# Performance work log

Measured on AMD Instinct MI355X. Metric: run time of the kernel, lower is better.

The kernel has to match this reference:

```python
import jax, jax.numpy as jnp
import numpy as np

N, C, H = 256, 128, 4
EPS = 1e-5


def setup_inputs() -> dict:
    key = jax.random.key(0)
    ks = jax.random.split(key, 12)
    def w(k, shape):
        return jax.random.normal(k, shape, jnp.float32) * 0.02
    return {
        'pair_rep': jax.random.normal(ks[0], (N, N, C), jnp.float32),
        'single_rep': jax.random.normal(ks[1], (N, C), jnp.float32),
        'mask': jax.random.randint(ks[2], (N, N), 0, 2) == 1,
        'distance_matrix': jax.random.normal(ks[3], (N, N), jnp.float32),
        'row_Wqkv': w(ks[4], (C, 3 * C)), 'row_bqkv': jnp.zeros((3 * C,), jnp.float32),
        'row_Wo': w(ks[5], (C, C)), 'row_bo': jnp.zeros((C,), jnp.float32),
        'row_dscale': jnp.ones((1,), jnp.float32),
        'col_Wqkv': w(ks[6], (C, 3 * C)), 'col_bqkv': jnp.zeros((3 * C,), jnp.float32),
        'col_Wo': w(ks[7], (C, C)), 'col_bo': jnp.zeros((C,), jnp.float32),
        'col_dscale': jnp.ones((1,), jnp.float32),
        'pnr_g': jnp.ones((C,), jnp.float32), 'pnr_b': jnp.zeros((C,), jnp.float32),
        'pnc_g': jnp.ones((C,), jnp.float32), 'pnc_b': jnp.zeros((C,), jnp.float32),
        'sn_g': jnp.ones((C,), jnp.float32), 'sn_b': jnp.zeros((C,), jnp.float32),
        'W1': w(ks[8], (C, 2 * C)), 'b1': jnp.zeros((2 * C,), jnp.float32),
        'W2': w(ks[9], (2 * C, C)), 'b2': jnp.zeros((C,), jnp.float32),
    }


def layer_norm(x, g, b):
    m = jnp.mean(x, axis=-1, keepdims=True)
    v = jnp.mean((x - m) ** 2, axis=-1, keepdims=True)
    return (x - m) / jnp.sqrt(v + EPS) * g + b


def tri_update_out(pair, single):
    # out[i,j] = single[j] + sum_{k<i} pair[i,k]  (exclusive prefix over own row, at index i)
    n = pair.shape[0]
    cs = jnp.cumsum(pair, axis=1)                       # cs[i,j] = sum_{k<=j} pair[i,k]
    idx = jnp.arange(n)
    s = cs[idx, jnp.maximum(idx - 1, 0)]                # [n,c]
    s = jnp.where((idx > 0)[:, None], s, 0.0)
    return single[None, :, :] + s[:, None, :]


def tri_update_in(pair, single):
    # out[i,j] = single[i] + sum_{k<j} pair[k,j]
    n = pair.shape[0]
    cs = jnp.cumsum(pair, axis=0)                       # cs[i,j] = sum_{k<=i} pair[k,j]
    idx = jnp.arange(n)
    s = cs[jnp.maximum(idx - 1, 0), idx]                # [n,c]
    s = jnp.where((idx > 0)[:, None], s, 0.0)
    return single[:, None, :] + s[None, :, :]


def tri_attn(x, Wqkv, bqkv, Wo, bo, dscale, mask, dist):
    n = x.shape[0]
    d = C // H
    qkv = x @ Wqkv + bqkv                               # [n,n,3c]
    q, k, v = jnp.split(qkv, 3, axis=-1)
    q = q.reshape(n, n, H, d)
    k = k.reshape(n, n, H, d)
    v = v.reshape(n, n, H, d)
    scores = jnp.einsum('ijhd,ikhd->hijk', q, k) / np.sqrt(d).astype(np.float32)
    scores = scores + (dscale[0] * dist)[None, None, :, :]
    scores = jnp.where(mask[None, None, :, :], -jnp.inf, scores)
    w = jax.nn.softmax(scores, axis=-1)
    out = jnp.einsum('hijk,ikhd->ijhd', w, v).reshape(n, n, C)
    return out @ Wo + bo


def reference(pair_rep, single_rep, mask, distance_matrix,
              row_Wqkv, row_bqkv, row_Wo, row_bo, row_dscale,
              col_Wqkv, col_bqkv, col_Wo, col_bo, col_dscale,
              pnr_g, pnr_b, pnc_g, pnc_b, sn_g, sn_b,
              W1, b1, W2, b2):
    pr = layer_norm(pair_rep + tri_update_out(pair_rep, single_rep), pnr_g, pnr_b)
    pr = layer_norm(pr + tri_attn(pr, row_Wqkv, row_bqkv, row_Wo, row_bo, row_dscale, mask, distance_matrix), pnr_g, pnr_b)
    pr = layer_norm(pr + tri_update_in(pr, single_rep), pnc_g, pnc_b)
    pr = layer_norm(pr + tri_attn(pr, col_Wqkv, col_bqkv, col_Wo, col_bo, col_dscale, mask.T, distance_matrix), pnc_g, pnc_b)
    h = jax.nn.relu(single_rep @ W1 + b1)
    h = jax.nn.relu(h @ W2 + b2)
    sr = layer_norm(single_rep + h, sn_g, sn_b)
    return pr, sr
```

## Files before the change

kernel.cpp:

```cpp
#include <hip/hip_runtime.h>
#include <math.h>

typedef unsigned int u32;
typedef unsigned short u16;
typedef __attribute__((ext_vector_type(8))) short short8;
typedef __attribute__((ext_vector_type(4))) float f32x4;
typedef __attribute__((ext_vector_type(2))) u32 u32x2;

#define NN 256
#define CC 128
#define EPSV 1e-5f
#define LOG2E 1.44269504088896f
#define QSCL (0.17677669529663687f * 1.44269504088896f)
#define NEGBIG -1e30f

#define MFMA(a,b,c) __builtin_amdgcn_mfma_f32_16x16x32_bf16(a,b,c,0,0,0)
#define EXP2(x) __builtin_amdgcn_exp2f(x)

__device__ __forceinline__ float b2f(u16 u){ return __uint_as_float(((u32)u)<<16); }
__device__ __forceinline__ u16 f2b(float f){
  u32 x = __float_as_uint(f);
  return (u16)((x + 0x7fffu + ((x>>16)&1u)) >> 16);
}
__device__ __forceinline__ void unpk(u32 u, float&a, float&b){
  a = __uint_as_float(u<<16); b = __uint_as_float(u & 0xffff0000u);
}
__device__ __forceinline__ u32 cvtpk(float lo, float hi){
  u32 r;
  asm("v_cvt_pk_bf16_f32 %0, %1, %2" : "=v"(r) : "v"(lo), "v"(hi));
  return r;
}

#define XS_OFF   0
#define WT_OFF   65536
#define WO_OFF   90112
#define KB_OFF   100352
#define VT_OFF   120832
#define PB_OFF   138752
#define SV_OFF   159232
#define GB_OFF   159744
#define SMEM_BYTES 161280

#define XBYTE(r,c) ((r)*256 + (((((c)>>3)) ^ ((r)&7))<<4) + ((c)&7)*2)

__global__ void bias_kernel(const int* __restrict__ mask, const float* __restrict__ dist,
                            const float* __restrict__ rd, const float* __restrict__ cd,
                            u16* __restrict__ b0, u16* __restrict__ b1){
  int j = blockIdx.x, k = threadIdx.x;
  float dv = dist[j*NN + k];
  b0[j*NN + k] = mask[j*NN + k] ? f2b(NEGBIG) : f2b(rd[0]*LOG2E*dv);
  b1[j*NN + k] = mask[k*NN + j] ? f2b(NEGBIG) : f2b(cd[0]*LOG2E*dv);
}

template<int PHASE, int BIASWS>
__launch_bounds__(1024, 4)
__global__ void stage_kernel(const float* __restrict__ pin, const float* __restrict__ colmat,
                             const float* __restrict__ singlerow,
                             const int* __restrict__ mask, const float* __restrict__ dist,
                             const u16* __restrict__ biasbuf,
                             const float* __restrict__ Wqkv, const float* __restrict__ bqkv,
                             const float* __restrict__ Wo, const float* __restrict__ bo,
                             const float* __restrict__ dscale,
                             const float* __restrict__ lng, const float* __restrict__ lnb,
                             float* __restrict__ outp)
{
  extern __shared__ char smem[];
  char* Xs  = smem + XS_OFF;
  char* WTs = smem + WT_OFF;
  char* WOs = smem + WO_OFF;
  char* KBs = smem + KB_OFF;
  char* VTs = smem + VT_OFF;
  float* SVs = (float*)(smem + SV_OFF);
  float* GBs = (float*)(smem + GB_OFF);

  const int i = blockIdx.x;
  const int tid = threadIdx.x;
  const int lid = tid & 63;
  const int w = tid >> 6;
  const int l15 = lid & 15;
  const int l4  = lid >> 4;
  char* pbB = smem + PB_OFF + w*1280;
  const float dsc = dscale[0] * LOG2E;
  const float* prow = pin + (size_t)i*NN*CC;
  float* orow = outp + (size_t)i*NN*CC;
  const int qglob = w*16 + l15;

  if (tid < CC){ GBs[tid] = lng[tid]; GBs[CC+tid] = lnb[tid]; GBs[2*CC+tid] = bo[tid]; }
  if (PHASE == 0) {
    float* REDp = (float*)(smem + PB_OFF);
    int c = tid & 127, part = tid >> 7;
    float acc = 0.f;
    for (int k = part; k < i; k += 8) acc += prow[k*CC + c];
    REDp[tid] = acc;
    __syncthreads();
    if (tid < CC){
      float s = 0.f;
      #pragma unroll
      for (int p = 0; p < 8; ++p) s += REDp[p*CC + tid];
      SVs[tid] = s;
    }
  } else {
    if (tid < CC) SVs[tid] = singlerow[i*CC + tid];
  }
  __syncthreads();

  for (int r = w; r < NN; r += 16){
    float t0 = prow[r*CC + lid]      + colmat[r*CC + lid]      + SVs[lid];
    float t1 = prow[r*CC + 64 + lid] + colmat[r*CC + 64 + lid] + SVs[64 + lid];
    float s = t0 + t1, q2 = t0*t0 + t1*t1;
    #pragma unroll
    for (int ms = 1; ms < 64; ms <<= 1){ s += __shfl_xor(s, ms); q2 += __shfl_xor(q2, ms); }
    float mean = s*(1.f/CC);
    float var  = fmaxf(q2*(1.f/CC) - mean*mean, 0.f);
    float rstd = rsqrtf(var + EPSV);
    *(u16*)(Xs + XBYTE(r, lid))    = f2b((t0-mean)*rstd*GBs[lid]    + GBs[CC+lid]);
    *(u16*)(Xs + XBYTE(r, 64+lid)) = f2b((t1-mean)*rstd*GBs[64+lid] + GBs[CC+64+lid]);
  }

  f32x4 pa[8];
  #pragma unroll
  for (int ct=0;ct<8;++ct) pa[ct] = f32x4{0.f,0.f,0.f,0.f};

  for (int h = 0; h < 4; ++h){
    __syncthreads();

    #pragma unroll
    for (int it = 0; it < 12; ++it){
      int e = tid + it*1024;
      int c = e & 127, t = e >> 7;
      int col = (t < 32) ? (h*32 + t) : (t < 64) ? (CC + h*32 + (t-32)) : (2*CC + h*32 + (t-64));
      *(u16*)(WTs + t*256 + ((((c>>3) ^ (t&7)))<<4) + (c&7)*2) = f2b(Wqkv[c*384 + col]);
    }
    #pragma unroll
    for (int it = 0; it < 4; ++it){
      int e = tid + it*1024;
      int d = e >> 7, o = e & 127;
      *(u16*)(WOs + (o*40 + d)*2) = f2b(Wo[(h*32 + d)*128 + o]);
    }
    __syncthreads();

    f32x4 qa[2], ka[2], va[2];
    {
      float bq0 = bqkv[h*32 + l15],      bq1 = bqkv[h*32 + 16 + l15];
      float bk0 = bqkv[CC + h*32 + l15], bk1 = bqkv[CC + h*32 + 16 + l15];
      qa[0] = f32x4{bq0,bq0,bq0,bq0}; qa[1] = f32x4{bq1,bq1,bq1,bq1};
      ka[0] = f32x4{bk0,bk0,bk0,bk0}; ka[1] = f32x4{bk1,bk1,bk1,bk1};
      #pragma unroll
      for (int dt=0;dt<2;++dt)
        #pragma unroll
        for (int v=0;v<4;++v) va[dt][v] = bqkv[2*CC + h*32 + dt*16 + l4*4 + v];
    }
    #pragma unroll
    for (int ks = 0; ks < 4; ++ks){
      int swb = (((ks*4 + l4) ^ (l15 & 7)) << 4);
      short8 a0  = *(const short8*)(Xs  + (w*16 + l15)*256 + swb);
      short8 wq0 = *(const short8*)(WTs + (l15)*256 + swb);
      short8 wq1 = *(const short8*)(WTs + (16 + l15)*256 + swb);
      short8 wk0 = *(const short8*)(WTs + (32 + l15)*256 + swb);
      short8 wk1 = *(const short8*)(WTs + (48 + l15)*256 + swb);
      short8 wv0 = *(const short8*)(WTs + (64 + l15)*256 + swb);
      short8 wv1 = *(const short8*)(WTs + (80 + l15)*256 + swb);
      qa[0]=MFMA(a0,wq0,qa[0]); qa[1]=MFMA(a0,wq1,qa[1]);
      ka[0]=MFMA(a0,wk0,ka[0]); ka[1]=MFMA(a0,wk1,ka[1]);
      va[0]=MFMA(wv0,a0,va[0]); va[1]=MFMA(wv1,a0,va[1]);
    }
    #pragma unroll
    for (int ct=0;ct<2;++ct)
      #pragma unroll
      for (int v=0;v<4;++v){
        *(u16*)(KBs + ((w*16 + l4*4 + v)*40 + ct*16 + l15)*2) = f2b(ka[ct][v]);
        *(u16*)(pbB + ((l4*4 + v)*40 + ct*16 + l15)*2) = f2b(qa[ct][v]*QSCL);
        *(u16*)(VTs + ((ct*16 + l4*4 + v)*280 + w*16 + l15)*2) = f2b(va[ct][v]);
      }
    asm volatile("s_waitcnt lgkmcnt(0)" ::: "memory");
    short8 qf = *(const short8*)(pbB + (l15)*80 + l4*16);
    __syncthreads();

    float m = -3e38f, l = 0.f;
    f32x4 oacc[2];
    oacc[0] = f32x4{0.f,0.f,0.f,0.f}; oacc[1] = oacc[0];

    #pragma unroll
    for (int ch = 0; ch < 8; ++ch){
      const int kbase = ch*32;
      float bia[2][4];
      if (BIASWS){
        u32x2 bw0 = *(const u32x2*)(biasbuf + qglob*NN + kbase + l4*4);
        u32x2 bw1 = *(const u32x2*)(biasbuf + qglob*NN + kbase + 16 + l4*4);
        unpk(bw0.x, bia[0][0], bia[0][1]); unpk(bw0.y, bia[0][2], bia[0][3]);
        unpk(bw1.x, bia[1][0], bia[1][1]); unpk(bw1.y, bia[1][2], bia[1][3]);
      } else {
        #pragma unroll
        for (int kt=0;kt<2;++kt)
          #pragma unroll
          for (int v=0;v<4;++v){
            int ky = kbase + kt*16 + l4*4 + v;
            int mq = (PHASE==0) ? mask[qglob*NN + ky] : mask[ky*NN + qglob];
            bia[kt][v] = mq ? NEGBIG : dsc*dist[qglob*NN + ky];
          }
      }
      short8 kf0 = *(const short8*)(KBs + (kbase + l15)*80 + l4*16);
      short8 kf1 = *(const short8*)(KBs + (kbase + 16 + l15)*80 + l4*16);
      f32x4 z = f32x4{0.f,0.f,0.f,0.f};
      f32x4 s0 = MFMA(kf0, qf, z);
      f32x4 s1 = MFMA(kf1, qf, z);
      float sv0 = s0[0]+bia[0][0], sv1 = s0[1]+bia[0][1], sv2 = s0[2]+bia[0][2], sv3 = s0[3]+bia[0][3];
      float sv4 = s1[0]+bia[1][0], sv5 = s1[1]+bia[1][1], sv6 = s1[2]+bia[1][2], sv7 = s1[3]+bia[1][3];
      float mx = fmaxf(fmaxf(fmaxf(sv0,sv1),fmaxf(sv2,sv3)), fmaxf(fmaxf(sv4,sv5),fmaxf(sv6,sv7)));
      mx = fmaxf(mx, __shfl_xor(mx, 16));
      mx = fmaxf(mx, __shfl_xor(mx, 32));
      float mn = fmaxf(m, mx);
      float corr = EXP2(m - mn);
      m = mn;
      float p00 = EXP2(sv0 - m), p01 = EXP2(sv1 - m), p02 = EXP2(sv2 - m), p03 = EXP2(sv3 - m);
      float p10 = EXP2(sv4 - m), p11 = EXP2(sv5 - m), p12 = EXP2(sv6 - m), p13 = EXP2(sv7 - m);
      float ps = ((p00+p01)+(p02+p03)) + ((p10+p11)+(p12+p13));
      ps += __shfl_xor(ps, 16);
      ps += __shfl_xor(ps, 32);
      l = l*corr + ps;
      #pragma unroll
      for (int v=0;v<4;++v){ oacc[0][v] *= corr; oacc[1][v] *= corr; }
      u32 A0 = cvtpk(p00,p01), A1 = cvtpk(p02,p03);
      u32 B0 = cvtpk(p10,p11), B1 = cvtpk(p12,p13);
      asm volatile("v_permlane32_swap_b32 %0, %1" : "+v"(A0), "+v"(B0));
      asm volatile("v_permlane32_swap_b32 %0, %1" : "+v"(A1), "+v"(B1));
      u32 sA0 = __shfl_xor(A0, 16), sA1 = __shfl_xor(A1, 16);
      u32 sB0 = __shfl_xor(B0, 16), sB1 = __shfl_xor(B1, 16);
      bool eg = ((l4 & 1) == 0);
      union { u32 u[4]; short8 s; } pu;
      pu.u[0] = eg ? A0 : sB0;
      pu.u[1] = eg ? A1 : sB1;
      pu.u[2] = eg ? sA0 : B0;
      pu.u[3] = eg ? sA1 : B1;
      short8 pf = pu.s;
      short8 vt0 = *(const short8*)(VTs + (l15)*560      + (kbase + l4*8)*2);
      short8 vt1 = *(const short8*)(VTs + (16 + l15)*560 + (kbase + l4*8)*2);
      oacc[0] = MFMA(vt0, pf, oacc[0]);
      oacc[1] = MFMA(vt1, pf, oacc[1]);
    }

    {
      float inv = 1.f / l;
      #pragma unroll
      for (int dt=0;dt<2;++dt)
        #pragma unroll
        for (int v=0;v<4;++v)
          *(u16*)(pbB + (l15*40 + dt*16 + l4*4 + v)*2) = f2b(oacc[dt][v]*inv);
      asm volatile("s_waitcnt lgkmcnt(0)" ::: "memory");
      short8 oA = *(const short8*)(pbB + (l15)*80 + l4*16);
      #pragma unroll
      for (int ct=0; ct<8; ++ct){
        short8 wB = *(const short8*)(WOs + (ct*16 + l15)*80 + l4*16);
        pa[ct] = MFMA(oA, wB, pa[ct]);
      }
    }
  }

  float mrs[4], mrq[4];
  #pragma unroll
  for (int v=0;v<4;++v){ mrs[v] = 0.f; mrq[v] = 0.f; }
  #pragma unroll
  for (int ct=0;ct<8;++ct)
    #pragma unroll
    for (int v=0;v<4;++v){
      int o = ct*16 + l15;
      int r = w*16 + l4*4 + v;
      float xv = b2f(*(const u16*)(Xs + XBYTE(r, o)));
      float t = pa[ct][v] + GBs[2*CC + o] + xv;
      pa[ct][v] = t;
      mrs[v] += t; mrq[v] += t*t;
    }
  #pragma unroll
  for (int v=0;v<4;++v){
    #pragma unroll
    for (int ms=1; ms<16; ms<<=1){
      mrs[v] += __shfl_xor(mrs[v], ms);
      mrq[v] += __shfl_xor(mrq[v], ms);
    }
    float mean = mrs[v]*(1.f/CC);
    float var  = fmaxf(mrq[v]*(1.f/CC) - mean*mean, 0.f);
    mrs[v] = mean;
    mrq[v] = rsqrtf(var + EPSV);
  }
  #pragma unroll
  for (int ct=0;ct<8;++ct)
    #pragma unroll
    for (int v=0;v<4;++v){
      int o = ct*16 + l15;
      int r = w*16 + l4*4 + v;
      orow[r*CC + o] = (pa[ct][v] - mrs[v])*mrq[v]*GBs[o] + GBs[CC+o];
    }
}

__launch_bounds__(512)
__global__ void colprefix_kernel(const float* __restrict__ pr, float* __restrict__ s_in){
  __shared__ float red[512];
  int j = blockIdx.x;
  int c = threadIdx.x & 127, part = threadIdx.x >> 7;
  float acc = 0.f;
  for (int k = part; k < j; k += 4) acc += pr[(size_t)k*NN*CC + j*CC + c];
  red[threadIdx.x] = acc;
  __syncthreads();
  if (threadIdx.x < 128)
    s_in[j*CC + threadIdx.x] = red[threadIdx.x] + red[128+threadIdx.x]
                             + red[256+threadIdx.x] + red[384+threadIdx.x];
}

__launch_bounds__(128)
__global__ void single_kernel(const float* __restrict__ single,
                              const float* __restrict__ W1, const float* __restrict__ b1,
                              const float* __restrict__ W2, const float* __restrict__ b2,
                              const float* __restrict__ g, const float* __restrict__ bb,
                              float* __restrict__ sr){
  __shared__ float srow[128];
  __shared__ float sh1[256];
  __shared__ float red[4];
  int jr = blockIdx.x, t = threadIdx.x;
  srow[t] = single[jr*CC + t];
  __syncthreads();
  float a0 = b1[t], a1 = b1[t+128];
  for (int c = 0; c < 128; ++c){
    float s = srow[c];
    a0 += s * W1[c*256 + t];
    a1 += s * W1[c*256 + t + 128];
  }
  sh1[t] = fmaxf(a0, 0.f);
  sh1[t+128] = fmaxf(a1, 0.f);
  __syncthreads();
  float acc = b2[t];
  for (int o = 0; o < 256; ++o) acc += sh1[o] * W2[o*CC + t];
  acc = fmaxf(acc, 0.f);
  float tv = srow[t] + acc;
  float s = tv, q = tv*tv;
  #pragma unroll
  for (int mm = 32; mm; mm >>= 1){ s += __shfl_xor(s, mm); q += __shfl_xor(q, mm); }
  int w = t >> 6;
  if ((t & 63) == 0){ red[w] = s; red[2+w] = q; }
  __syncthreads();
  float S = red[0] + red[1], Q = red[2] + red[3];
  float mean = S*(1.f/CC);
  float var = fmaxf(Q*(1.f/CC) - mean*mean, 0.f);
  float rs = rsqrtf(var + EPSV);
  sr[jr*CC + t] = (tv - mean)*rs*g[t] + bb[t];
}

extern "C" void kernel_launch(void* const* d_in, const int* in_sizes, int n_in,
                              void* d_out, int out_size, void* d_ws, size_t ws_size,
                              hipStream_t stream) {
  const float* pair   = (const float*)d_in[0];
  const float* single = (const float*)d_in[1];
  const int*   mask   = (const int*)d_in[2];
  const float* dist   = (const float*)d_in[3];
  const float* rWqkv  = (const float*)d_in[4];
  const float* rbqkv  = (const float*)d_in[5];
  const float* rWo    = (const float*)d_in[6];
  const float* rbo    = (const float*)d_in[7];
  const float* rdsc   = (const float*)d_in[8];
  const float* cWqkv  = (const float*)d_in[9];
  const float* cbqkv  = (const float*)d_in[10];
  const float* cWo    = (const float*)d_in[11];
  const float* cbo    = (const float*)d_in[12];
  const float* cdsc   = (const float*)d_in[13];
  const float* pnr_g  = (const float*)d_in[14];
  const float* pnr_b  = (const float*)d_in[15];
  const float* pnc_g  = (const float*)d_in[16];
  const float* pnc_b  = (const float*)d_in[17];
  const float* sn_g   = (const float*)d_in[18];
  const float* sn_b   = (const float*)d_in[19];
  const float* W1     = (const float*)d_in[20];
  const float* b1     = (const float*)d_in[21];
  const float* W2     = (const float*)d_in[22];
  const float* b2     = (const float*)d_in[23];

  float* outp = (float*)d_out;
  float* pr   = outp;
  float* srr  = outp + (size_t)NN*NN*CC;

  const size_t ws_need = (size_t)NN*NN*2*2 + (size_t)NN*CC*4;
  const bool usews = ws_size >= ws_need;
  u16* bias0 = (u16*)d_ws;
  u16* bias1 = bias0 + NN*NN;
  float* s_in = usews ? (float*)((char*)d_ws + (size_t)NN*NN*4) : srr;

  if (usews){
    (void)hipFuncSetAttribute(reinterpret_cast<const void*>(stage_kernel<0,1>),
                              hipFuncAttributeMaxDynamicSharedMemorySize, SMEM_BYTES);
    (void)hipFuncSetAttribute(reinterpret_cast<const void*>(stage_kernel<1,1>),
                              hipFuncAttributeMaxDynamicSharedMemorySize, SMEM_BYTES);
    bias_kernel<<<NN, NN, 0, stream>>>(mask, dist, rdsc, cdsc, bias0, bias1);
    stage_kernel<0,1><<<NN, 1024, SMEM_BYTES, stream>>>(pair, single, single, mask, dist, bias0,
        rWqkv, rbqkv, rWo, rbo, rdsc, pnr_g, pnr_b, pr);
    colprefix_kernel<<<NN, 512, 0, stream>>>(pr, s_in);
    stage_kernel<1,1><<<NN, 1024, SMEM_BYTES, stream>>>(pr, s_in, single, mask, dist, bias1,
        cWqkv, cbqkv, cWo, cbo, cdsc, pnc_g, pnc_b, pr);
  } else {
    (void)hipFuncSetAttribute(reinterpret_cast<const void*>(stage_kernel<0,0>),
                              hipFuncAttributeMaxDynamicSharedMemorySize, SMEM_BYTES);
    (void)hipFuncSetAttribute(reinterpret_cast<const void*>(stage_kernel<1,0>),
                              hipFuncAttributeMaxDynamicSharedMemorySize, SMEM_BYTES);
    stage_kernel<0,0><<<NN, 1024, SMEM_BYTES, stream>>>(pair, single, single, mask, dist, nullptr,
        rWqkv, rbqkv, rWo, rbo, rdsc, pnr_g, pnr_b, pr);
    colprefix_kernel<<<NN, 512, 0, stream>>>(pr, s_in);
    stage_kernel<1,0><<<NN, 1024, SMEM_BYTES, stream>>>(pr, s_in, single, mask, dist, nullptr,
        cWqkv, cbqkv, cWo, cbo, cdsc, pnc_g, pnc_b, pr);
  }
  single_kernel<<<NN, CC, 0, stream>>>(single, W1, b1, W2, b2, sn_g, sn_b, srr);
}
```

Baseline: 293.4 us.

## Pre-pack weights and bias images, async-load into LDS, keep Q and P in registers

A prep kernel now converts the per-head QKV and output weights once into a bf16, LDS-ready image in workspace. Each stage block streams that image into LDS with global_load_lds and prefetches the next head's weights while the current head's attention runs, double-buffering Wo. The bias is stored in a layout that allows 16-byte vector loads. Q and the attention output are redistributed in registers with permlane and shuffle instead of round-tripping through LDS. The layer-norm prologue is vectorized to float4 and fused with the row prefix sum, the attention loop is restructured into two halves of four chunks, and colprefix uses 1024 threads with nontemporal loads and stores. In exchange the change adds an extra launch and more workspace, and the async-copy path is more complex.

```diff
diff --git a/kernel.cpp b/kernel.cpp
--- a/kernel.cpp
+++ b/kernel.cpp
@@ -30,34 +30,83 @@
   asm("v_cvt_pk_bf16_f32 %0, %1, %2" : "=v"(r) : "v"(lo), "v"(hi));
   return r;
 }
+__device__ __forceinline__ void gload16(const void* g, void* l){
+  __builtin_amdgcn_global_load_lds((const __attribute__((address_space(1))) u32*)g,
+                                   (__attribute__((address_space(3))) u32*)l, 16, 0, 0);
+}
+
+__device__ __forceinline__ short8 redist(f32x4 t0, f32x4 t1, int l4){
+  u32 A0 = cvtpk(t0[0], t0[1]), A1 = cvtpk(t0[2], t0[3]);
+  u32 B0 = cvtpk(t1[0], t1[1]), B1 = cvtpk(t1[2], t1[3]);
+  asm volatile("v_permlane32_swap_b32 %0, %1" : "+v"(A0), "+v"(B0));
+  asm volatile("v_permlane32_swap_b32 %0, %1" : "+v"(A1), "+v"(B1));
+  u32 sA0 = __shfl_xor(A0, 16), sA1 = __shfl_xor(A1, 16);
+  u32 sB0 = __shfl_xor(B0, 16), sB1 = __shfl_xor(B1, 16);
+  bool eg = ((l4 & 1) == 0);
+  union { u32 u[4]; short8 s; } pu;
+  pu.u[0] = eg ? A0 : sB0;
+  pu.u[1] = eg ? A1 : sB1;
+  pu.u[2] = eg ? sA0 : B0;
+  pu.u[3] = eg ? sA1 : B1;
+  return pu.s;
+}
 
 #define XS_OFF   0
 #define WT_OFF   65536
 #define WO_OFF   90112
-#define KB_OFF   100352
-#define VT_OFF   120832
-#define PB_OFF   138752
-#define SV_OFF   159232
-#define GB_OFF   159744
-#define SMEM_BYTES 161280
+#define KB_OFF   110592
+#define VT_OFF   131072
+#define SV_OFF   147968
+#define GB_OFF   148480
+#define BQ_OFF   150016
+#define RS_OFF   151552
+#define SMEM_BYTES 159744
 
 #define XBYTE(r,c) ((r)*256 + (((((c)>>3)) ^ ((r)&7))<<4) + ((c)&7)*2)
 
-__global__ void bias_kernel(const int* __restrict__ mask, const float* __restrict__ dist,
-                            const float* __restrict__ rd, const float* __restrict__ cd,
-                            u16* __restrict__ b0, u16* __restrict__ b1){
-  int j = blockIdx.x, k = threadIdx.x;
-  float dv = dist[j*NN + k];
-  b0[j*NN + k] = mask[j*NN + k] ? f2b(NEGBIG) : f2b(rd[0]*LOG2E*dv);
-  b1[j*NN + k] = mask[k*NN + j] ? f2b(NEGBIG) : f2b(cd[0]*LOG2E*dv);
-}
-
-template<int PHASE, int BIASWS>
+#define WS_B0   0
+#define WS_B1   131072
+#define WS_W0   262144
+#define WS_W1   401408
+#define WS_SIN  540672
+#define WS_NEED 671744
+
+__global__ void prep_bias(const int* __restrict__ mask, const float* __restrict__ dist,
+                          const float* __restrict__ rd, const float* __restrict__ cd,
+                          u16* __restrict__ b0, u16* __restrict__ b1){
+  int q = blockIdx.x, k = threadIdx.x;
+  int l4 = (k >> 2) & 3, v = k & 3, kt = (k >> 4) & 1, ch = k >> 5;
+  int addr = q*256 + l4*64 + ch*8 + kt*4 + v;
+  float dv = dist[q*NN + k];
+  b0[addr] = mask[q*NN + k] ? f2b(NEGBIG) : f2b(rd[0]*LOG2E*dv);
+  b1[addr] = mask[k*NN + q] ? f2b(NEGBIG) : f2b(cd[0]*LOG2E*dv);
+}
+
+__global__ void prep_wimg(const float* __restrict__ rWqkv, const float* __restrict__ rWo,
+                          const float* __restrict__ cWqkv, const float* __restrict__ cWo,
+                          u16* __restrict__ img0, u16* __restrict__ img1){
+  int h = blockIdx.x & 3, s = blockIdx.x >> 2;
+  const float* Wq = s ? cWqkv : rWqkv;
+  const float* Wom = s ? cWo : rWo;
+  char* base = (char*)(s ? img1 : img0) + h*34816;
+  for (int e = threadIdx.x; e < 96*128; e += 256){
+    int t = e >> 7, c = e & 127;
+    int col = (t < 32) ? (h*32 + t) : (t < 64) ? (CC + h*32 + (t-32)) : (2*CC + h*32 + (t-64));
+    *(u16*)(base + t*256 + ((((c>>3) ^ (t&7)))<<4) + (c&7)*2) = f2b(Wq[c*384 + col]);
+  }
+  for (int e = threadIdx.x; e < 128*40; e += 256){
+    int o = e / 40, d = e - o*40;
+    *(u16*)(base + 24576 + (o*40 + d)*2) = (d < 32) ? f2b(Wom[(h*32 + d)*128 + o]) : (u16)0;
+  }
+}
+
+template<int PHASE, int WSOK>
 __launch_bounds__(1024, 4)
 __global__ void stage_kernel(const float* __restrict__ pin, const float* __restrict__ colmat,
                              const float* __restrict__ singlerow,
                              const int* __restrict__ mask, const float* __restrict__ dist,
-                             const u16* __restrict__ biasbuf,
+                             const u16* __restrict__ biasimg,
+                             const u16* __restrict__ wimg,
                              const float* __restrict__ Wqkv, const float* __restrict__ bqkv,
                              const float* __restrict__ Wo, const float* __restrict__ bo,
                              const float* __restrict__ dscale,
@@ -72,6 +121,8 @@
   char* VTs = smem + VT_OFF;
   float* SVs = (float*)(smem + SV_OFF);
   float* GBs = (float*)(smem + GB_OFF);
+  float* BQs = (float*)(smem + BQ_OFF);
+  float* RSs = (float*)(smem + RS_OFF);
 
   const int i = blockIdx.x;
   const int tid = threadIdx.x;
@@ -79,76 +130,133 @@
   const int w = tid >> 6;
   const int l15 = lid & 15;
   const int l4  = lid >> 4;
-  char* pbB = smem + PB_OFF + w*1280;
-  const float dsc = dscale[0] * LOG2E;
+  const int h32 = lid >> 5;
+  const int c4  = (lid & 31) * 4;
   const float* prow = pin + (size_t)i*NN*CC;
   float* orow = outp + (size_t)i*NN*CC;
   const int qglob = w*16 + l15;
-
-  if (tid < CC){ GBs[tid] = lng[tid]; GBs[CC+tid] = lnb[tid]; GBs[2*CC+tid] = bo[tid]; }
-  if (PHASE == 0) {
-    float* REDp = (float*)(smem + PB_OFF);
-    int c = tid & 127, part = tid >> 7;
-    float acc = 0.f;
-    for (int k = part; k < i; k += 8) acc += prow[k*CC + c];
-    REDp[tid] = acc;
+  const float dsc = dscale[0] * LOG2E;
+
+  if (WSOK){
+    const char* wb = (const char*)wimg;
+    gload16(wb + tid*16, WTs + tid*16);
+    if (tid < 512) gload16(wb + 16384 + tid*16, WTs + 16384 + tid*16);
+    if (tid < 640) gload16(wb + 24576 + tid*16, WOs + tid*16);
+  }
+  if (tid < 128){ GBs[tid] = lng[tid]; GBs[128+tid] = lnb[tid]; GBs[256+tid] = bo[tid]; }
+  if (tid >= 512 && tid < 896) BQs[tid-512] = bqkv[tid-512];
+
+  if (PHASE == 0){
+    f32x4 svp = {0.f,0.f,0.f,0.f};
+    #pragma unroll 4
+    for (int p = 0; p < 8; ++p){
+      int r = w*16 + p*2 + h32;
+      f32x4 pr4 = __builtin_nontemporal_load((const f32x4*)(prow + r*CC + c4));
+      f32x4 sg4 = *(const f32x4*)(colmat + r*CC + c4);
+      f32x4 t = pr4 + sg4;
+      u32x2 pk2; pk2.x = cvtpk(t[0], t[1]); pk2.y = cvtpk(t[2], t[3]);
+      *(u32x2*)(Xs + XBYTE(r, c4)) = pk2;
+      if (r < i) svp += pr4;
+    }
+    #pragma unroll
+    for (int q = 0; q < 4; ++q) svp[q] += __shfl_xor(svp[q], 32);
+    if (h32 == 0) *(f32x4*)(RSs + w*128 + c4) = svp;
     __syncthreads();
-    if (tid < CC){
+    if (tid < 128){
       float s = 0.f;
       #pragma unroll
-      for (int p = 0; p < 8; ++p) s += REDp[p*CC + tid];
+      for (int ww = 0; ww < 16; ++ww) s += RSs[ww*128 + tid];
       SVs[tid] = s;
     }
+    __syncthreads();
+    f32x4 sv4 = *(const f32x4*)(SVs + c4);
+    f32x4 g4  = *(const f32x4*)(GBs + c4);
+    f32x4 b4  = *(const f32x4*)(GBs + 128 + c4);
+    #pragma unroll 2
+    for (int p = 0; p < 8; ++p){
+      int r = w*16 + p*2 + h32;
+      u32x2 st = *(const u32x2*)(Xs + XBYTE(r, c4));
+      float t0,t1,t2,t3;
+      unpk(st.x, t0, t1); unpk(st.y, t2, t3);
+      t0 += sv4[0]; t1 += sv4[1]; t2 += sv4[2]; t3 += sv4[3];
+      float s = (t0+t1)+(t2+t3);
+      float q2 = (t0*t0+t1*t1)+(t2*t2+t3*t3);
+      #pragma unroll
+      for (int ms = 1; ms < 32; ms <<= 1){ s += __shfl_xor(s, ms); q2 += __shfl_xor(q2, ms); }
+      float mean = s*(1.f/CC);
+      float var  = fmaxf(q2*(1.f/CC) - mean*mean, 0.f);
+      float rstd = rsqrtf(var + EPSV);
+      float y0 = (t0-mean)*rstd*g4[0] + b4[0];
+      float y1 = (t1-mean)*rstd*g4[1] + b4[1];
+      float y2 = (t2-mean)*rstd*g4[2] + b4[2];
+      float y3 = (t3-mean)*rstd*g4[3] + b4[3];
+      u32x2 pk2; pk2.x = cvtpk(y0, y1); pk2.y = cvtpk(y2, y3);
+      *(u32x2*)(Xs + XBYTE(r, c4)) = pk2;
+    }
   } else {
-    if (tid < CC) SVs[tid] = singlerow[i*CC + tid];
-  }
+    if (tid < 128) SVs[tid] = singlerow[i*CC + tid];
+    __syncthreads();
+    f32x4 sv4 = *(const f32x4*)(SVs + c4);
+    f32x4 g4  = *(const f32x4*)(GBs + c4);
+    f32x4 b4  = *(const f32x4*)(GBs + 128 + c4);
+    #pragma unroll 4
+    for (int p = 0; p < 8; ++p){
+      int r = w*16 + p*2 + h32;
+      f32x4 pr4 = __builtin_nontemporal_load((const f32x4*)(prow + r*CC + c4));
+      f32x4 cm4 = *(const f32x4*)(colmat + r*CC + c4);
+      float t0 = pr4[0]+cm4[0]+sv4[0], t1 = pr4[1]+cm4[1]+sv4[1];
+      float t2 = pr4[2]+cm4[2]+sv4[2], t3 = pr4[3]+cm4[3]+sv4[3];
+      float s = (t0+t1)+(t2+t3);
+      float q2 = (t0*t0+t1*t1)+(t2*t2+t3*t3);
+      #pragma unroll
+      for (int ms = 1; ms < 32; ms <<= 1){ s += __shfl_xor(s, ms); q2 += __shfl_xor(q2, ms); }
+      float mean = s*(1.f/CC);
+      float var  = fmaxf(q2*(1.f/CC) - mean*mean, 0.f);
+      float rstd = rsqrtf(var + EPSV);
+      float y0 = (t0-mean)*rstd*g4[0] + b4[0];
+      float y1 = (t1-mean)*rstd*g4[1] + b4[1];
+      float y2 = (t2-mean)*rstd*g4[2] + b4[2];
+      float y3 = (t3-mean)*rstd*g4[3] + b4[3];
+      u32x2 pk2; pk2.x = cvtpk(y0, y1); pk2.y = cvtpk(y2, y3);
+      *(u32x2*)(Xs + XBYTE(r, c4)) = pk2;
+    }
+  }
+  if (WSOK) asm volatile("s_waitcnt vmcnt(0)" ::: "memory");
   __syncthreads();
-
-  for (int r = w; r < NN; r += 16){
-    float t0 = prow[r*CC + lid]      + colmat[r*CC + lid]      + SVs[lid];
-    float t1 = prow[r*CC + 64 + lid] + colmat[r*CC + 64 + lid] + SVs[64 + lid];
-    float s = t0 + t1, q2 = t0*t0 + t1*t1;
-    #pragma unroll
-    for (int ms = 1; ms < 64; ms <<= 1){ s += __shfl_xor(s, ms); q2 += __shfl_xor(q2, ms); }
-    float mean = s*(1.f/CC);
-    float var  = fmaxf(q2*(1.f/CC) - mean*mean, 0.f);
-    float rstd = rsqrtf(var + EPSV);
-    *(u16*)(Xs + XBYTE(r, lid))    = f2b((t0-mean)*rstd*GBs[lid]    + GBs[CC+lid]);
-    *(u16*)(Xs + XBYTE(r, 64+lid)) = f2b((t1-mean)*rstd*GBs[64+lid] + GBs[CC+64+lid]);
-  }
 
   f32x4 pa[8];
   #pragma unroll
-  for (int ct=0;ct<8;++ct) pa[ct] = f32x4{0.f,0.f,0.f,0.f};
+  for (int ct = 0; ct < 8; ++ct) pa[ct] = f32x4{0.f,0.f,0.f,0.f};
 
   for (int h = 0; h < 4; ++h){
-    __syncthreads();
-
-    #pragma unroll
-    for (int it = 0; it < 12; ++it){
-      int e = tid + it*1024;
-      int c = e & 127, t = e >> 7;
-      int col = (t < 32) ? (h*32 + t) : (t < 64) ? (CC + h*32 + (t-32)) : (2*CC + h*32 + (t-64));
-      *(u16*)(WTs + t*256 + ((((c>>3) ^ (t&7)))<<4) + (c&7)*2) = f2b(Wqkv[c*384 + col]);
-    }
-    #pragma unroll
-    for (int it = 0; it < 4; ++it){
-      int e = tid + it*1024;
-      int d = e >> 7, o = e & 127;
-      *(u16*)(WOs + (o*40 + d)*2) = f2b(Wo[(h*32 + d)*128 + o]);
-    }
-    __syncthreads();
+    if (!WSOK){
+      #pragma unroll
+      for (int it = 0; it < 12; ++it){
+        int e = tid + it*1024;
+        int c = e & 127, t = e >> 7;
+        int col = (t < 32) ? (h*32 + t) : (t < 64) ? (CC + h*32 + (t-32)) : (2*CC + h*32 + (t-64));
+        *(u16*)(WTs + t*256 + ((((c>>3) ^ (t&7)))<<4) + (c&7)*2) = f2b(Wqkv[c*384 + col]);
+      }
+      #pragma unroll
+      for (int it = 0; it < 4; ++it){
+        int e = tid + it*1024;
+        int d = e >> 7, o = e & 127;
+        *(u16*)(WOs + (h&1)*10240 + (o*40 + d)*2) = (d < 32) ? f2b(Wo[(h*32 + d)*128 + o]) : (u16)0;
+      }
+      __syncthreads();
+    }
 
     f32x4 qa[2], ka[2], va[2];
+    #pragma unroll
+    for (int dt = 0; dt < 2; ++dt)
+      #pragma unroll
+      for (int v = 0; v < 4; ++v){
+        qa[dt][v] = BQs[h*32 + dt*16 + l4*4 + v];
+        va[dt][v] = BQs[256 + h*32 + dt*16 + l4*4 + v];
+      }
     {
-      float bq0 = bqkv[h*32 + l15],      bq1 = bqkv[h*32 + 16 + l15];
-      float bk0 = bqkv[CC + h*32 + l15], bk1 = bqkv[CC + h*32 + 16 + l15];
-      qa[0] = f32x4{bq0,bq0,bq0,bq0}; qa[1] = f32x4{bq1,bq1,bq1,bq1};
+      float bk0 = BQs[128 + h*32 + l15], bk1 = BQs[128 + h*32 + 16 + l15];
       ka[0] = f32x4{bk0,bk0,bk0,bk0}; ka[1] = f32x4{bk1,bk1,bk1,bk1};
-      #pragma unroll
-      for (int dt=0;dt<2;++dt)
-        #pragma unroll
-        for (int v=0;v<4;++v) va[dt][v] = bqkv[2*CC + h*32 + dt*16 + l4*4 + v];
     }
     #pragma unroll
     for (int ks = 0; ks < 4; ++ks){
@@ -160,120 +268,138 @@
       short8 wk1 = *(const short8*)(WTs + (48 + l15)*256 + swb);
       short8 wv0 = *(const short8*)(WTs + (64 + l15)*256 + swb);
       short8 wv1 = *(const short8*)(WTs + (80 + l15)*256 + swb);
-      qa[0]=MFMA(a0,wq0,qa[0]); qa[1]=MFMA(a0,wq1,qa[1]);
-      ka[0]=MFMA(a0,wk0,ka[0]); ka[1]=MFMA(a0,wk1,ka[1]);
-      va[0]=MFMA(wv0,a0,va[0]); va[1]=MFMA(wv1,a0,va[1]);
-    }
-    #pragma unroll
-    for (int ct=0;ct<2;++ct)
-      #pragma unroll
-      for (int v=0;v<4;++v){
-        *(u16*)(KBs + ((w*16 + l4*4 + v)*40 + ct*16 + l15)*2) = f2b(ka[ct][v]);
-        *(u16*)(pbB + ((l4*4 + v)*40 + ct*16 + l15)*2) = f2b(qa[ct][v]*QSCL);
-        *(u16*)(VTs + ((ct*16 + l4*4 + v)*280 + w*16 + l15)*2) = f2b(va[ct][v]);
-      }
-    asm volatile("s_waitcnt lgkmcnt(0)" ::: "memory");
-    short8 qf = *(const short8*)(pbB + (l15)*80 + l4*16);
+      qa[0] = MFMA(wq0, a0, qa[0]); qa[1] = MFMA(wq1, a0, qa[1]);
+      ka[0] = MFMA(a0, wk0, ka[0]); ka[1] = MFMA(a0, wk1, ka[1]);
+      va[0] = MFMA(wv0, a0, va[0]); va[1] = MFMA(wv1, a0, va[1]);
+    }
+    short8 qf = redist(qa[0]*QSCL, qa[1]*QSCL, l4);
+    #pragma unroll
+    for (int kt = 0; kt < 2; ++kt)
+      #pragma unroll
+      for (int v = 0; v < 4; ++v)
+        *(u16*)(KBs + ((w*16 + l4*4 + v)*40 + kt*16 + l15)*2) = (u16)cvtpk(ka[kt][v], ka[kt][v]);
+    #pragma unroll
+    for (int dt = 0; dt < 2; ++dt)
+      #pragma unroll
+      for (int v = 0; v < 4; ++v)
+        *(u16*)(VTs + ((dt*16 + l4*4 + v)*264 + w*16 + l15)*2) = (u16)cvtpk(va[dt][v], va[dt][v]);
     __syncthreads();
 
+    if (WSOK && h < 3){
+      const char* wb = (const char*)wimg + (h+1)*34816;
+      gload16(wb + tid*16, WTs + tid*16);
+      if (tid < 512) gload16(wb + 16384 + tid*16, WTs + 16384 + tid*16);
+      if (tid < 640) gload16(wb + 24576 + tid*16, WOs + ((h+1)&1)*10240 + tid*16);
+    }
+
     float m = -3e38f, l = 0.f;
-    f32x4 oacc[2];
-    oacc[0] = f32x4{0.f,0.f,0.f,0.f}; oacc[1] = oacc[0];
-
-    #pragma unroll
-    for (int ch = 0; ch < 8; ++ch){
-      const int kbase = ch*32;
-      float bia[2][4];
-      if (BIASWS){
-        u32x2 bw0 = *(const u32x2*)(biasbuf + qglob*NN + kbase + l4*4);
-        u32x2 bw1 = *(const u32x2*)(biasbuf + qglob*NN + kbase + 16 + l4*4);
-        unpk(bw0.x, bia[0][0], bia[0][1]); unpk(bw0.y, bia[0][2], bia[0][3]);
-        unpk(bw1.x, bia[1][0], bia[1][1]); unpk(bw1.y, bia[1][2], bia[1][3]);
+    f32x4 oacc0 = {0.f,0.f,0.f,0.f}, oacc1 = {0.f,0.f,0.f,0.f};
+    #pragma unroll
+    for (int hl = 0; hl < 2; ++hl){
+      f32x4 sS[4][2];
+      #pragma unroll
+      for (int ci = 0; ci < 4; ++ci){
+        int ch = hl*4 + ci;
+        short8 kf0 = *(const short8*)(KBs + (ch*32 + l15)*80 + l4*16);
+        short8 kf1 = *(const short8*)(KBs + (ch*32 + 16 + l15)*80 + l4*16);
+        f32x4 z = {0.f,0.f,0.f,0.f};
+        sS[ci][0] = MFMA(kf0, qf, z);
+        sS[ci][1] = MFMA(kf1, qf, z);
+      }
+      if (WSOK){
+        const u16* bb = biasimg + qglob*256 + l4*64 + hl*32;
+        #pragma unroll
+        for (int ci = 0; ci < 4; ++ci){
+          uint4 bw = *(const uint4*)(bb + ci*8);
+          float b00,b01,b02,b03,b10,b11,b12,b13;
+          unpk(bw.x, b00, b01); unpk(bw.y, b02, b03);
+          unpk(bw.z, b10, b11); unpk(bw.w, b12, b13);
+          sS[ci][0][0]+=b00; sS[ci][0][1]+=b01; sS[ci][0][2]+=b02; sS[ci][0][3]+=b03;
+          sS[ci][1][0]+=b10; sS[ci][1][1]+=b11; sS[ci][1][2]+=b12; sS[ci][1][3]+=b13;
+        }
       } else {
         #pragma unroll
-        for (int kt=0;kt<2;++kt)
+        for (int ci = 0; ci < 4; ++ci)
           #pragma unroll
-          for (int v=0;v<4;++v){
-            int ky = kbase + kt*16 + l4*4 + v;
-            int mq = (PHASE==0) ? mask[qglob*NN + ky] : mask[ky*NN + qglob];
-            bia[kt][v] = mq ? NEGBIG : dsc*dist[qglob*NN + ky];
-          }
-      }
-      short8 kf0 = *(const short8*)(KBs + (kbase + l15)*80 + l4*16);
-      short8 kf1 = *(const short8*)(KBs + (kbase + 16 + l15)*80 + l4*16);
-      f32x4 z = f32x4{0.f,0.f,0.f,0.f};
-      f32x4 s0 = MFMA(kf0, qf, z);
-      f32x4 s1 = MFMA(kf1, qf, z);
-      float sv0 = s0[0]+bia[0][0], sv1 = s0[1]+bia[0][1], sv2 = s0[2]+bia[0][2], sv3 = s0[3]+bia[0][3];
-      float sv4 = s1[0]+bia[1][0], sv5 = s1[1]+bia[1][1], sv6 = s1[2]+bia[1][2], sv7 = s1[3]+bia[1][3];
-      float mx = fmaxf(fmaxf(fmaxf(sv0,sv1),fmaxf(sv2,sv3)), fmaxf(fmaxf(sv4,sv5),fmaxf(sv6,sv7)));
+          for (int kt = 0; kt < 2; ++kt)
+            #pragma unroll
+            for (int v = 0; v < 4; ++v){
+              int key = (hl*4 + ci)*32 + kt*16 + l4*4 + v;
+              int mq = (PHASE==0) ? mask[qglob*NN + key] : mask[key*NN + qglob];
+              sS[ci][kt][v] += mq ? NEGBIG : dsc*dist[qglob*NN + key];
+            }
+      }
+      float mc0 = fmaxf(fmaxf(fmaxf(sS[0][0][0],sS[0][0][1]),fmaxf(sS[0][0][2],sS[0][0][3])),
+                        fmaxf(fmaxf(sS[0][1][0],sS[0][1][1]),fmaxf(sS[0][1][2],sS[0][1][3])));
+      float mc1 = fmaxf(fmaxf(fmaxf(sS[1][0][0],sS[1][0][1]),fmaxf(sS[1][0][2],sS[1][0][3])),
+                        fmaxf(fmaxf(sS[1][1][0],sS[1][1][1]),fmaxf(sS[1][1][2],sS[1][1][3])));
+      float mc2 = fmaxf(fmaxf(fmaxf(sS[2][0][0],sS[2][0][1]),fmaxf(sS[2][0][2],sS[2][0][3])),
+                        fmaxf(fmaxf(sS[2][1][0],sS[2][1][1]),fmaxf(sS[2][1][2],sS[2][1][3])));
+      float mc3 = fmaxf(fmaxf(fmaxf(sS[3][0][0],sS[3][0][1]),fmaxf(sS[3][0][2],sS[3][0][3])),
+                        fmaxf(fmaxf(sS[3][1][0],sS[3][1][1]),fmaxf(sS[3][1][2],sS[3][1][3])));
+      float mx = fmaxf(fmaxf(mc0,mc1), fmaxf(mc2,mc3));
       mx = fmaxf(mx, __shfl_xor(mx, 16));
       mx = fmaxf(mx, __shfl_xor(mx, 32));
       float mn = fmaxf(m, mx);
       float corr = EXP2(m - mn);
       m = mn;
-      float p00 = EXP2(sv0 - m), p01 = EXP2(sv1 - m), p02 = EXP2(sv2 - m), p03 = EXP2(sv3 - m);
-      float p10 = EXP2(sv4 - m), p11 = EXP2(sv5 - m), p12 = EXP2(sv6 - m), p13 = EXP2(sv7 - m);
-      float ps = ((p00+p01)+(p02+p03)) + ((p10+p11)+(p12+p13));
+      float ps = 0.f;
+      #pragma unroll
+      for (int ci = 0; ci < 4; ++ci){
+        float p0=0.f, p1=0.f;
+        #pragma unroll
+        for (int v = 0; v < 4; ++v){
+          sS[ci][0][v] = EXP2(sS[ci][0][v] - m); p0 += sS[ci][0][v];
+          sS[ci][1][v] = EXP2(sS[ci][1][v] - m); p1 += sS[ci][1][v];
+        }
+        ps += p0 + p1;
+      }
       ps += __shfl_xor(ps, 16);
       ps += __shfl_xor(ps, 32);
       l = l*corr + ps;
-      #pragma unroll
-      for (int v=0;v<4;++v){ oacc[0][v] *= corr; oacc[1][v] *= corr; }
-      u32 A0 = cvtpk(p00,p01), A1 = cvtpk(p02,p03);
-      u32 B0 = cvtpk(p10,p11), B1 = cvtpk(p12,p13);
-      asm volatile("v_permlane32_swap_b32 %0, %1" : "+v"(A0), "+v"(B0));
-      asm volatile("v_permlane32_swap_b32 %0, %1" : "+v"(A1), "+v"(B1));
-      u32 sA0 = __shfl_xor(A0, 16), sA1 = __shfl_xor(A1, 16);
-      u32 sB0 = __shfl_xor(B0, 16), sB1 = __shfl_xor(B1, 16);
-      bool eg = ((l4 & 1) == 0);
-      union { u32 u[4]; short8 s; } pu;
-      pu.u[0] = eg ? A0 : sB0;
-      pu.u[1] = eg ? A1 : sB1;
-      pu.u[2] = eg ? sA0 : B0;
-      pu.u[3] = eg ? sA1 : B1;
-      short8 pf = pu.s;
-      short8 vt0 = *(const short8*)(VTs + (l15)*560      + (kbase + l4*8)*2);
-      short8 vt1 = *(const short8*)(VTs + (16 + l15)*560 + (kbase + l4*8)*2);
-      oacc[0] = MFMA(vt0, pf, oacc[0]);
-      oacc[1] = MFMA(vt1, pf, oacc[1]);
-    }
-
+      oacc0 *= corr; oacc1 *= corr;
+      #pragma unroll
+      for (int ci = 0; ci < 4; ++ci){
+        int ch = hl*4 + ci;
+        short8 pf = redist(sS[ci][0], sS[ci][1], l4);
+        short8 vt0 = *(const short8*)(VTs + (l15)*528 + ch*64 + l4*16);
+        short8 vt1 = *(const short8*)(VTs + (16 + l15)*528 + ch*64 + l4*16);
+        oacc0 = MFMA(vt0, pf, oacc0);
+        oacc1 = MFMA(vt1, pf, oacc1);
+      }
+    }
     {
       float inv = 1.f / l;
-      #pragma unroll
-      for (int dt=0;dt<2;++dt)
-        #pragma unroll
-        for (int v=0;v<4;++v)
-          *(u16*)(pbB + (l15*40 + dt*16 + l4*4 + v)*2) = f2b(oacc[dt][v]*inv);
-      asm volatile("s_waitcnt lgkmcnt(0)" ::: "memory");
-      short8 oA = *(const short8*)(pbB + (l15)*80 + l4*16);
-      #pragma unroll
-      for (int ct=0; ct<8; ++ct){
-        short8 wB = *(const short8*)(WOs + (ct*16 + l15)*80 + l4*16);
+      short8 oA = redist(oacc0*inv, oacc1*inv, l4);
+      const char* wob = WOs + (h&1)*10240;
+      #pragma unroll
+      for (int ct = 0; ct < 8; ++ct){
+        short8 wB = *(const short8*)(wob + (ct*16 + l15)*80 + l4*16);
         pa[ct] = MFMA(oA, wB, pa[ct]);
       }
     }
+    if (WSOK && h < 3) asm volatile("s_waitcnt vmcnt(0)" ::: "memory");
+    __syncthreads();
   }
 
   float mrs[4], mrq[4];
   #pragma unroll
-  for (int v=0;v<4;++v){ mrs[v] = 0.f; mrq[v] = 0.f; }
+  for (int v = 0; v < 4; ++v){ mrs[v] = 0.f; mrq[v] = 0.f; }
   #pragma unroll
-  for (int ct=0;ct<8;++ct)
-    #pragma unroll
-    for (int v=0;v<4;++v){
+  for (int ct = 0; ct < 8; ++ct)
+    #pragma unroll
+    for (int v = 0; v < 4; ++v){
       int o = ct*16 + l15;
       int r = w*16 + l4*4 + v;
       float xv = b2f(*(const u16*)(Xs + XBYTE(r, o)));
-      float t = pa[ct][v] + GBs[2*CC + o] + xv;
+      float t = pa[ct][v] + GBs[256 + o] + xv;
       pa[ct][v] = t;
       mrs[v] += t; mrq[v] += t*t;
     }
   #pragma unroll
-  for (int v=0;v<4;++v){
-    #pragma unroll
-    for (int ms=1; ms<16; ms<<=1){
+  for (int v = 0; v < 4; ++v){
+    #pragma unroll
+    for (int ms = 1; ms < 16; ms <<= 1){
       mrs[v] += __shfl_xor(mrs[v], ms);
       mrq[v] += __shfl_xor(mrq[v], ms);
     }
@@ -283,27 +409,32 @@
     mrq[v] = rsqrtf(var + EPSV);
   }
   #pragma unroll
-  for (int ct=0;ct<8;++ct)
-    #pragma unroll
-    for (int v=0;v<4;++v){
+  for (int ct = 0; ct < 8; ++ct)
+    #pragma unroll
+    for (int v = 0; v < 4; ++v){
       int o = ct*16 + l15;
       int r = w*16 + l4*4 + v;
-      orow[r*CC + o] = (pa[ct][v] - mrs[v])*mrq[v]*GBs[o] + GBs[CC+o];
-    }
-}
-
-__launch_bounds__(512)
+      __builtin_nontemporal_store((pa[ct][v] - mrs[v])*mrq[v]*GBs[o] + GBs[128+o],
+                                  orow + r*CC + o);
+    }
+}
+
+__launch_bounds__(1024)
 __global__ void colprefix_kernel(const float* __restrict__ pr, float* __restrict__ s_in){
-  __shared__ float red[512];
+  __shared__ float red[1024];
   int j = blockIdx.x;
   int c = threadIdx.x & 127, part = threadIdx.x >> 7;
   float acc = 0.f;
-  for (int k = part; k < j; k += 4) acc += pr[(size_t)k*NN*CC + j*CC + c];
+  for (int k = part; k < j; k += 8)
+    acc += __builtin_nontemporal_load(pr + (size_t)k*NN*CC + j*CC + c);
   red[threadIdx.x] = acc;
   __syncthreads();
-  if (threadIdx.x < 128)
-    s_in[j*CC + threadIdx.x] = red[threadIdx.x] + red[128+threadIdx.x]
-                             + red[256+threadIdx.x] + red[384+threadIdx.x];
+  if (threadIdx.x < 128){
+    float s = 0.f;
+    #pragma unroll
+    for (int p = 0; p < 8; ++p) s += red[p*128 + threadIdx.x];
+    s_in[j*CC + threadIdx.x] = s;
+  }
 }
 
 __launch_bounds__(128)
@@ -376,33 +507,36 @@
   float* pr   = outp;
   float* srr  = outp + (size_t)NN*NN*CC;
 
-  const size_t ws_need = (size_t)NN*NN*2*2 + (size_t)NN*CC*4;
-  const bool usews = ws_size >= ws_need;
-  u16* bias0 = (u16*)d_ws;
-  u16* bias1 = bias0 + NN*NN;
-  float* s_in = usews ? (float*)((char*)d_ws + (size_t)NN*NN*4) : srr;
+  const bool usews = ws_size >= (size_t)WS_NEED;
+  char* wsb = (char*)d_ws;
+  u16* bias0 = (u16*)(wsb + WS_B0);
+  u16* bias1 = (u16*)(wsb + WS_B1);
+  u16* wimg0 = (u16*)(wsb + WS_W0);
+  u16* wimg1 = (u16*)(wsb + WS_W1);
+  float* s_in = usews ? (float*)(wsb + WS_SIN) : srr;
 
   if (usews){
     (void)hipFuncSetAttribute(reinterpret_cast<const void*>(stage_kernel<0,1>),
                               hipFuncAttributeMaxDynamicSharedMemorySize, SMEM_BYTES);
     (void)hipFuncSetAttribute(reinterpret_cast<const void*>(stage_kernel<1,1>),
                               hipFuncAttributeMaxDynamicSharedMemorySize, SMEM_BYTES);
-    bias_kernel<<<NN, NN, 0, stream>>>(mask, dist, rdsc, cdsc, bias0, bias1);
-    stage_kernel<0,1><<<NN, 1024, SMEM_BYTES, stream>>>(pair, single, single, mask, dist, bias0,
-        rWqkv, rbqkv, rWo, rbo, rdsc, pnr_g, pnr_b, pr);
-    colprefix_kernel<<<NN, 512, 0, stream>>>(pr, s_in);
-    stage_kernel<1,1><<<NN, 1024, SMEM_BYTES, stream>>>(pr, s_in, single, mask, dist, bias1,
-        cWqkv, cbqkv, cWo, cbo, cdsc, pnc_g, pnc_b, pr);
+    prep_bias<<<NN, NN, 0, stream>>>(mask, dist, rdsc, cdsc, bias0, bias1);
+    prep_wimg<<<8, 256, 0, stream>>>(rWqkv, rWo, cWqkv, cWo, wimg0, wimg1);
+    stage_kernel<0,1><<<NN, 1024, SMEM_BYTES, stream>>>(pair, single, single, mask, dist,
+        bias0, wimg0, rWqkv, rbqkv, rWo, rbo, rdsc, pnr_g, pnr_b, pr);
+    colprefix_kernel<<<NN, 1024, 0, stream>>>(pr, s_in);
+    stage_kernel<1,1><<<NN, 1024, SMEM_BYTES, stream>>>(pr, s_in, single, mask, dist,
+        bias1, wimg1, cWqkv, cbqkv, cWo, cbo, cdsc, pnc_g, pnc_b, pr);
   } else {
     (void)hipFuncSetAttribute(reinterpret_cast<const void*>(stage_kernel<0,0>),
                               hipFuncAttributeMaxDynamicSharedMemorySize, SMEM_BYTES);
     (void)hipFuncSetAttribute(reinterpret_cast<const void*>(stage_kernel<1,0>),
                               hipFuncAttributeMaxDynamicSharedMemorySize, SMEM_BYTES);
-    stage_kernel<0,0><<<NN, 1024, SMEM_BYTES, stream>>>(pair, single, single, mask, dist, nullptr,
-        rWqkv, rbqkv, rWo, rbo, rdsc, pnr_g, pnr_b, pr);
-    colprefix_kernel<<<NN, 512, 0, stream>>>(pr, s_in);
-    stage_kernel<1,0><<<NN, 1024, SMEM_BYTES, stream>>>(pr, s_in, single, mask, dist, nullptr,
-        cWqkv, cbqkv, cWo, cbo, cdsc, pnc_g, pnc_b, pr);
+    stage_kernel<0,0><<<NN, 1024, SMEM_BYTES, stream>>>(pair, single, single, mask, dist,
+        nullptr, nullptr, rWqkv, rbqkv, rWo, rbo, rdsc, pnr_g, pnr_b, pr);
+    colprefix_kernel<<<NN, 1024, 0, stream>>>(pr, s_in);
+    stage_kernel<1,0><<<NN, 1024, SMEM_BYTES, stream>>>(pr, s_in, single, mask, dist,
+        nullptr, nullptr, cWqkv, cbqkv, cWo, cbo, cdsc, pnc_g, pnc_b, pr);
   }
   single_kernel<<<NN, CC, 0, stream>>>(single, W1, b1, W2, b2, sn_g, sn_b, srr);
 }
```

New measurement: 282.6 us. 3.7% less time.
